# Performance work log

Hardware: AMD Instinct MI355X
Metric: run time of the kernel (lower is better)

Reference implementation:

```python
import jax, jax.numpy as jnp
import numpy as np

COMMITMENT_COST = 0.25


def setup_inputs() -> dict:
    key = jax.random.key(0)
    k1, k2 = jax.random.split(key)
    inputs = jax.random.normal(k1, (64, 1024, 128), dtype=jnp.float32)
    # torch.rand init -> uniform [0, 1)
    codewords = jax.random.uniform(k2, (1024, 128), dtype=jnp.float32)
    return {"inputs": inputs, "codewords": codewords}


def reference(inputs, codewords):
    sg = jax.lax.stop_gradient
    D = codewords.shape[-1]
    flat = inputs.reshape(-1, D)  # (N, D)
    distances = (
        jnp.sum(flat * flat, axis=1, keepdims=True)
        - 2.0 * flat @ codewords.T
        + jnp.sum(codewords * codewords, axis=1)
    )  # (N, K)
    encoding_indices = jnp.argmin(distances, axis=1)  # (N,)
    quantized = codewords[encoding_indices].reshape(inputs.shape)

    quantizing_loss = jnp.mean((sg(quantized) - inputs) ** 2)
    commitment_loss = jnp.mean((quantized - sg(inputs)) ** 2)
    loss = quantizing_loss + COMMITMENT_COST * commitment_loss

    # straight-through estimator
    quantized = inputs + sg(quantized - inputs)
    return quantized, encoding_indices[:, None], loss
```

## Files before the change

### kernel.cpp

```cpp
#include <hip/hip_runtime.h>
#include <stdint.h>


typedef short     bf16x8 __attribute__((ext_vector_type(8)));
typedef float     f32x4  __attribute__((ext_vector_type(4)));
typedef unsigned short u16x8 __attribute__((ext_vector_type(8)));
typedef unsigned short u16x2 __attribute__((ext_vector_type(2)));

constexpr int N_ROWS = 65536;
constexpr int K_CODES = 1024;
constexpr int D = 128;
constexpr float MARGIN = 0.01f;

__device__ __forceinline__ unsigned short f32_to_bf16_rn(float f) {
    unsigned u = __float_as_uint(f);
    unsigned r = (u + 0x7FFFu + ((u >> 16) & 1u)) >> 16;
    return (unsigned short)r;
}
__device__ __forceinline__ float bf16_to_f32(unsigned short h) {
    return __uint_as_float(((unsigned)h) << 16);
}

__device__ __forceinline__ void gload_lds16(const void* g, void* l) {
    __builtin_amdgcn_global_load_lds(
        (const __attribute__((address_space(1))) unsigned int*)g,
        (__attribute__((address_space(3))) unsigned int*)l, 16, 0, 0);
}

__global__ __launch_bounds__(64) void vq_prep_cw(const float* __restrict__ cw,
                                                 unsigned short* __restrict__ Cp,
                                                 float* __restrict__ cnorm,
                                                 int* __restrict__ rcnt,
                                                 double* __restrict__ acc) {
    const int k = blockIdx.x;
    const int lane = threadIdx.x;
    float2 v = reinterpret_cast<const float2*>(cw + (size_t)k * D)[lane];
    float s = v.x * v.x + v.y * v.y;
#pragma unroll
    for (int off = 32; off; off >>= 1) s += __shfl_down(s, off, 64);
    if (lane == 0) cnorm[k] = s;
    if (lane == 0 && k == 0) { *rcnt = 0; *acc = 0.0; }

    unsigned short hx = f32_to_bf16_rn(v.x), hy = f32_to_bf16_rn(v.y);
    unsigned short lx = f32_to_bf16_rn(v.x - bf16_to_f32(hx));
    unsigned short ly = f32_to_bf16_rn(v.y - bf16_to_f32(hy));
    size_t off0 = (size_t)k * D + lane * 2;
    u16x2 hv; hv[0] = hx; hv[1] = hy;
    u16x2 lv; lv[0] = lx; lv[1] = ly;
    *reinterpret_cast<u16x2*>(Cp + off0) = hv;
    *reinterpret_cast<u16x2*>(Cp + 131072 + off0) = lv;
}

__global__ __launch_bounds__(256, 2) void vq_argmin_fused(
    const float* __restrict__ x,
    const unsigned short* __restrict__ Cp,
    const float* __restrict__ cnorm,
    const float* __restrict__ cw,
    float* __restrict__ out_idx_f,
    float* __restrict__ qout,
    float* __restrict__ rowloss,
    float* __restrict__ xnorm,
    int* __restrict__ rcnt,
    int* __restrict__ rrows,
    double* __restrict__ acc) {
    __shared__ unsigned char Bs[2][2][16384];
    __shared__ int idx_s[128];
    __shared__ float xs_n[128];
    __shared__ double wsum[4];

    const int tid = threadIdx.x;
    const int wave = tid >> 6;
    const int lane = tid & 63;
    const int l15 = lane & 15;
    const int lg = lane >> 4;
    const int base = blockIdx.x * 128;
    const int wrow = base + wave * 32;

    const char* Cpb = reinterpret_cast<const char*>(Cp);
    auto stageB = [&](int c, int b) {
#pragma unroll
        for (int u = 0; u < 8; ++u) {
            int t = wave * 8 + u;
            int pl = t >> 4;
            int cwl = (t & 15) * 4 + lg;
            int q = l15 * 16;
            const char* src = Cpb + pl * 262144 + ((size_t)(c * 64 + cwl)) * 256
                              + (q ^ ((cwl & 7) << 4));
            void* dst = (void*)&Bs[b][pl][(t & 15) * 1024];
            gload_lds16(src, dst);
        }
    };
    stageB(0, 0);

    bf16x8 A[2][4][2];
    float xn[2] = {0.f, 0.f};
#pragma unroll
    for (int r2 = 0; r2 < 2; ++r2) {
        const float* xr0 = x + (size_t)(wrow + r2 * 16 + l15) * D;
#pragma unroll
        for (int s = 0; s < 4; ++s) {
            const float4* xf = reinterpret_cast<const float4*>(xr0 + s * 32 + lg * 8);
            float4 f0 = xf[0];
            float4 f1 = xf[1];
            float in[8] = {f0.x, f0.y, f0.z, f0.w, f1.x, f1.y, f1.z, f1.w};
            u16x8 hv, lv;
#pragma unroll
            for (int e = 0; e < 8; ++e) {
                xn[r2] += in[e] * in[e];
                unsigned short h = f32_to_bf16_rn(in[e]);
                hv[e] = h;
                lv[e] = f32_to_bf16_rn(in[e] - bf16_to_f32(h));
            }
            A[r2][s][0] = *reinterpret_cast<bf16x8*>(&hv);
            A[r2][s][1] = *reinterpret_cast<bf16x8*>(&lv);
        }
    }
#pragma unroll
    for (int r2 = 0; r2 < 2; ++r2) {
        xn[r2] += __shfl_xor(xn[r2], 16, 64);
        xn[r2] += __shfl_xor(xn[r2], 32, 64);
        if (lg == 0) {
            xs_n[wave * 32 + r2 * 16 + l15] = xn[r2];
            xnorm[wrow + r2 * 16 + l15] = xn[r2];
        }
    }

    float bv[2][4], bv2[2][4];
    int bi_[2][4];
#pragma unroll
    for (int r2 = 0; r2 < 2; ++r2)
#pragma unroll
        for (int i = 0; i < 4; ++i) { bv[r2][i] = 3.4e38f; bv2[r2][i] = 3.4e38f; bi_[r2][i] = 0; }

    const int cb = l15 * 256;
    const int swz = (l15 & 7) << 4;
    int kb[4];
#pragma unroll
    for (int s = 0; s < 4; ++s) kb[s] = (s * 64 + lg * 16) ^ swz;

    asm volatile("s_waitcnt vmcnt(0)" ::: "memory");
    __syncthreads();

    for (int c = 0; c < 16; ++c) {
        const int buf = c & 1;
        if (c < 15) stageB(c + 1, buf ^ 1);

        f32x4 accf[2][4];
#pragma unroll
        for (int r2 = 0; r2 < 2; ++r2)
#pragma unroll
            for (int j = 0; j < 4; ++j) accf[r2][j] = (f32x4)(0.f);

#pragma unroll
        for (int s = 0; s < 4; ++s) {
            bf16x8 bh[4], bl[4];
#pragma unroll
            for (int j = 0; j < 4; ++j) {
                int ad = j * 4096 + cb + kb[s];
                bh[j] = *reinterpret_cast<const bf16x8*>(&Bs[buf][0][ad]);
                bl[j] = *reinterpret_cast<const bf16x8*>(&Bs[buf][1][ad]);
            }
#pragma unroll
            for (int r2 = 0; r2 < 2; ++r2)
#pragma unroll
                for (int j = 0; j < 4; ++j) {
                    accf[r2][j] = __builtin_amdgcn_mfma_f32_16x16x32_bf16(
                        A[r2][s][0], bh[j], accf[r2][j], 0, 0, 0);
                    accf[r2][j] = __builtin_amdgcn_mfma_f32_16x16x32_bf16(
                        A[r2][s][0], bl[j], accf[r2][j], 0, 0, 0);
                    accf[r2][j] = __builtin_amdgcn_mfma_f32_16x16x32_bf16(
                        A[r2][s][1], bh[j], accf[r2][j], 0, 0, 0);
                }
        }

#pragma unroll
        for (int j = 0; j < 4; ++j) {
            int col = c * 64 + j * 16 + l15;
            float cn = cnorm[col];
#pragma unroll
            for (int r2 = 0; r2 < 2; ++r2)
#pragma unroll
                for (int i = 0; i < 4; ++i) {
                    float sc = cn - 2.f * accf[r2][j][i];
                    if (sc < bv[r2][i]) {
                        bv2[r2][i] = bv[r2][i];
                        bv[r2][i] = sc;
                        bi_[r2][i] = col;
                    } else if (sc < bv2[r2][i]) {
                        bv2[r2][i] = sc;
                    }
                }
        }
        asm volatile("s_waitcnt vmcnt(0)" ::: "memory");
        __syncthreads();
    }

    double lsum = 0.0;
#pragma unroll
    for (int r2 = 0; r2 < 2; ++r2)
#pragma unroll
        for (int i = 0; i < 4; ++i) {
            float v = bv[r2][i], v2 = bv2[r2][i];
            int ix = bi_[r2][i];
#pragma unroll
            for (int off = 1; off < 16; off <<= 1) {
                float ov = __shfl_xor(v, off, 64);
                float ov2 = __shfl_xor(v2, off, 64);
                int oi = __shfl_xor(ix, off, 64);
                float nv2 = fminf(fminf(v2, ov2), fmaxf(v, ov));
                if (ov < v || (ov == v && oi < ix)) { v = ov; ix = oi; }
                v2 = nv2;
            }
            if (l15 == 0) {
                int rl_loc = wave * 32 + r2 * 16 + lg * 4 + i;
                int row = base + rl_loc;
                out_idx_f[row] = (float)ix;
                idx_s[rl_loc] = ix;
                float rl = xs_n[rl_loc] + v;
                rowloss[row] = rl;
                lsum += (double)rl;
                if (v2 - v < MARGIN) {
                    int p = atomicAdd(rcnt, 1);
                    rrows[p] = row;
                }
            }
        }

#pragma unroll
    for (int off = 32; off; off >>= 1) lsum += __shfl_down(lsum, off, 64);
    if (lane == 0) wsum[wave] = lsum;
    __syncthreads();
    if (tid == 0) atomicAdd(acc, wsum[0] + wsum[1] + wsum[2] + wsum[3]);

    const float4* cw4 = reinterpret_cast<const float4*>(cw);
    float4* q4 = reinterpret_cast<float4*>(qout);
#pragma unroll
    for (int it = 0; it < 16; ++it) {
        int i = it * 256 + tid;
        int r = i >> 5, d4 = i & 31;
        q4[(size_t)(base + r) * 32 + d4] = cw4[(size_t)idx_s[r] * 32 + d4];
    }
}

__global__ __launch_bounds__(256) void vq_repair(const float* __restrict__ x,
                                                 const float* __restrict__ cw,
                                                 const float* __restrict__ cnorm,
                                                 const float* __restrict__ xnorm,
                                                 const int* __restrict__ rcnt,
                                                 const int* __restrict__ rrows,
                                                 float* __restrict__ out_idx_f,
                                                 float* __restrict__ qout,
                                                 float* __restrict__ rowloss,
                                                 double* __restrict__ acc) {
    __shared__ float xs[16][132];
    __shared__ int rowids[16];
    __shared__ float sval[16][16];
    __shared__ int sidx[16][16];
    __shared__ int fidx[16];

    const int t = threadIdx.x;
    const int count = *rcnt;
    const float4* cw4 = reinterpret_cast<const float4*>(cw);
    double dsum = 0.0;

    for (int g = blockIdx.x; g * 16 < count; g += 512) {
        int nrows = min(16, count - g * 16);
        __syncthreads();
        if (t < 16) rowids[t] = rrows[g * 16 + (t < nrows ? t : 0)];
        __syncthreads();
        for (int i = t; i < 512; i += 256) {
            int r = i >> 5, d4 = i & 31;
            *reinterpret_cast<float4*>(&xs[r][d4 * 4]) =
                reinterpret_cast<const float4*>(x)[(size_t)rowids[r] * 32 + d4];
        }
        __syncthreads();

        const int r = t & 15;
        const int qq = t >> 4;
        float bv = 3.4e38f;
        int bi = 0;
#pragma unroll 2
        for (int kt = 0; kt < 8; ++kt) {
            float a[8] = {0.f, 0.f, 0.f, 0.f, 0.f, 0.f, 0.f, 0.f};
            int k0 = qq * 64 + kt * 8;
            for (int d4 = 0; d4 < 32; ++d4) {
                float4 xv = *reinterpret_cast<const float4*>(&xs[r][d4 * 4]);
#pragma unroll
                for (int kk = 0; kk < 8; ++kk) {
                    float4 cv = cw4[(size_t)(k0 + kk) * 32 + d4];
                    a[kk] += xv.x * cv.x + xv.y * cv.y + xv.z * cv.z + xv.w * cv.w;
                }
            }
#pragma unroll
            for (int kk = 0; kk < 8; ++kk) {
                int k = k0 + kk;
                float sc = cnorm[k] - 2.f * a[kk];
                if (sc < bv) { bv = sc; bi = k; }
            }
        }
        sval[r][qq] = bv;
        sidx[r][qq] = bi;
        __syncthreads();
        if (t < 16) {
            float fv = sval[t][0];
            int fi = sidx[t][0];
#pragma unroll
            for (int q2 = 1; q2 < 16; ++q2) {
                float v = sval[t][q2];
                int ii = sidx[t][q2];
                if (v < fv || (v == fv && ii < fi)) { fv = v; fi = ii; }
            }
            fidx[t] = fi;
            if (t < nrows) {
                int row = rowids[t];
                out_idx_f[row] = (float)fi;
                float nrl = xnorm[row] + fv;
                float orl = rowloss[row];
                rowloss[row] = nrl;
                dsum += (double)nrl - (double)orl;
            }
        }
        __syncthreads();
        for (int i = t; i < 512; i += 256) {
            int rr = i >> 5, d4 = i & 31;
            float4 q4 = cw4[(size_t)fidx[rr] * 32 + d4];
            reinterpret_cast<float4*>(qout)[(size_t)rowids[rr] * 32 + d4] = q4;
        }
    }
#pragma unroll
    for (int off = 32; off; off >>= 1) dsum += __shfl_down(dsum, off, 64);
    __shared__ double wsum[4];
    if ((t & 63) == 0) wsum[t >> 6] = dsum;
    __syncthreads();
    if (t == 0) {
        double b = wsum[0] + wsum[1] + wsum[2] + wsum[3];
        if (b != 0.0) atomicAdd(acc, b);
    }
}

__global__ void vq_loss_final(const double* __restrict__ acc,
                              float* __restrict__ out_loss) {
    *out_loss = (float)(*acc * (1.25 / (double)((size_t)N_ROWS * D)));
}

extern "C" void kernel_launch(void* const* d_in, const int* in_sizes, int n_in,
                              void* d_out, int out_size, void* d_ws, size_t ws_size,
                              hipStream_t stream) {
    const float* x = (const float*)d_in[0];
    const float* cw = (const float*)d_in[1];

    float* qout = (float*)d_out;
    float* out_idx_f = qout + (size_t)N_ROWS * D;
    float* out_loss = out_idx_f + N_ROWS;

    char* w = (char*)d_ws;
    unsigned short* Cp = (unsigned short*)w;          w += 524288;
    float* cnorm = (float*)w;                         w += 4096;
    int* rcnt = (int*)w;                              w += 16;
    double* acc = (double*)w;                         w += 240;
    int* rrows = (int*)w;                             w += 262144;
    float* xnorm = (float*)w;                         w += 262144;
    float* rowloss = (float*)w;                       w += 262144;

    vq_prep_cw<<<K_CODES, 64, 0, stream>>>(cw, Cp, cnorm, rcnt, acc);
    vq_argmin_fused<<<N_ROWS / 128, 256, 0, stream>>>(
        x, Cp, cnorm, cw, out_idx_f, qout, rowloss, xnorm, rcnt, rrows, acc);
    vq_repair<<<512, 256, 0, stream>>>(
        x, cw, cnorm, xnorm, rcnt, rrows, out_idx_f, qout, rowloss, acc);
    vq_loss_final<<<1, 1, 0, stream>>>(acc, out_loss);
}
```

Baseline: 225.7 us.

## Split codeword columns across two wave groups per block with 512 threads

Doubles the block to 512 threads. Each row group of 4 waves is duplicated, and each copy handles half of every 64-codeword chunk (32 columns). Per-wave top-2 results go through shared memory and are merged by the first 128 threads, which then write the index, loss and repair flags. The aim is more waves per CU and fewer accumulator registers per wave, to raise occupancy and hide MFMA and LDS latency. The cost is that both halves redundantly load and split x into bf16, plus an extra shared-memory merge step and barrier.

```diff
diff --git a/kernel.cpp b/kernel.cpp
--- a/kernel.cpp
+++ b/kernel.cpp
@@ -51,7 +51,7 @@
     *reinterpret_cast<u16x2*>(Cp + 131072 + off0) = lv;
 }
 
-__global__ __launch_bounds__(256, 2) void vq_argmin_fused(
+__global__ __launch_bounds__(512, 4) void vq_argmin_fused(
     const float* __restrict__ x,
     const unsigned short* __restrict__ Cp,
     const float* __restrict__ cnorm,
@@ -64,23 +64,27 @@
     int* __restrict__ rrows,
     double* __restrict__ acc) {
     __shared__ unsigned char Bs[2][2][16384];
+    __shared__ float mv[2][128], mv2[2][128];
+    __shared__ int mi[2][128];
     __shared__ int idx_s[128];
     __shared__ float xs_n[128];
-    __shared__ double wsum[4];
+    __shared__ double wsum[8];
 
     const int tid = threadIdx.x;
     const int wave = tid >> 6;
     const int lane = tid & 63;
     const int l15 = lane & 15;
     const int lg = lane >> 4;
+    const int rg = wave & 3;
+    const int ch = wave >> 2;
     const int base = blockIdx.x * 128;
-    const int wrow = base + wave * 32;
+    const int wrow = base + rg * 32;
 
     const char* Cpb = reinterpret_cast<const char*>(Cp);
     auto stageB = [&](int c, int b) {
 #pragma unroll
-        for (int u = 0; u < 8; ++u) {
-            int t = wave * 8 + u;
+        for (int u = 0; u < 4; ++u) {
+            int t = wave * 4 + u;
             int pl = t >> 4;
             int cwl = (t & 15) * 4 + lg;
             int q = l15 * 16;
@@ -119,18 +123,24 @@
     for (int r2 = 0; r2 < 2; ++r2) {
         xn[r2] += __shfl_xor(xn[r2], 16, 64);
         xn[r2] += __shfl_xor(xn[r2], 32, 64);
-        if (lg == 0) {
-            xs_n[wave * 32 + r2 * 16 + l15] = xn[r2];
+        if (ch == 0 && lg == 0) {
+            xs_n[rg * 32 + r2 * 16 + l15] = xn[r2];
             xnorm[wrow + r2 * 16 + l15] = xn[r2];
         }
     }
 
-    float bv[2][4], bv2[2][4];
-    int bi_[2][4];
+    float bv[2][2], bv2[2][2];
+    int bi_[2][2];
 #pragma unroll
     for (int r2 = 0; r2 < 2; ++r2)
 #pragma unroll
-        for (int i = 0; i < 4; ++i) { bv[r2][i] = 3.4e38f; bv2[r2][i] = 3.4e38f; bi_[r2][i] = 0; }
+        for (int i = 0; i < 2; ++i) {}
+    float tv[2][4], tv2[2][4];
+    int ti[2][4];
+#pragma unroll
+    for (int r2 = 0; r2 < 2; ++r2)
+#pragma unroll
+        for (int i = 0; i < 4; ++i) { tv[r2][i] = 3.4e38f; tv2[r2][i] = 3.4e38f; ti[r2][i] = 0; }
 
     const int cb = l15 * 256;
     const int swz = (l15 & 7) << 4;
@@ -145,25 +155,25 @@
         const int buf = c & 1;
         if (c < 15) stageB(c + 1, buf ^ 1);
 
-        f32x4 accf[2][4];
+        f32x4 accf[2][2];
 #pragma unroll
         for (int r2 = 0; r2 < 2; ++r2)
 #pragma unroll
-            for (int j = 0; j < 4; ++j) accf[r2][j] = (f32x4)(0.f);
+            for (int j = 0; j < 2; ++j) accf[r2][j] = (f32x4)(0.f);
 
 #pragma unroll
         for (int s = 0; s < 4; ++s) {
-            bf16x8 bh[4], bl[4];
-#pragma unroll
-            for (int j = 0; j < 4; ++j) {
-                int ad = j * 4096 + cb + kb[s];
+            bf16x8 bh[2], bl[2];
+#pragma unroll
+            for (int j = 0; j < 2; ++j) {
+                int ad = (ch * 2 + j) * 4096 + cb + kb[s];
                 bh[j] = *reinterpret_cast<const bf16x8*>(&Bs[buf][0][ad]);
                 bl[j] = *reinterpret_cast<const bf16x8*>(&Bs[buf][1][ad]);
             }
 #pragma unroll
             for (int r2 = 0; r2 < 2; ++r2)
 #pragma unroll
-                for (int j = 0; j < 4; ++j) {
+                for (int j = 0; j < 2; ++j) {
                     accf[r2][j] = __builtin_amdgcn_mfma_f32_16x16x32_bf16(
                         A[r2][s][0], bh[j], accf[r2][j], 0, 0, 0);
                     accf[r2][j] = __builtin_amdgcn_mfma_f32_16x16x32_bf16(
@@ -174,20 +184,20 @@
         }
 
 #pragma unroll
-        for (int j = 0; j < 4; ++j) {
-            int col = c * 64 + j * 16 + l15;
+        for (int j = 0; j < 2; ++j) {
+            int col = c * 64 + (ch * 2 + j) * 16 + l15;
             float cn = cnorm[col];
 #pragma unroll
             for (int r2 = 0; r2 < 2; ++r2)
 #pragma unroll
                 for (int i = 0; i < 4; ++i) {
                     float sc = cn - 2.f * accf[r2][j][i];
-                    if (sc < bv[r2][i]) {
-                        bv2[r2][i] = bv[r2][i];
-                        bv[r2][i] = sc;
-                        bi_[r2][i] = col;
-                    } else if (sc < bv2[r2][i]) {
-                        bv2[r2][i] = sc;
+                    if (sc < tv[r2][i]) {
+                        tv2[r2][i] = tv[r2][i];
+                        tv[r2][i] = sc;
+                        ti[r2][i] = col;
+                    } else if (sc < tv2[r2][i]) {
+                        tv2[r2][i] = sc;
                     }
                 }
         }
@@ -195,13 +205,12 @@
         __syncthreads();
     }
 
-    double lsum = 0.0;
 #pragma unroll
     for (int r2 = 0; r2 < 2; ++r2)
 #pragma unroll
         for (int i = 0; i < 4; ++i) {
-            float v = bv[r2][i], v2 = bv2[r2][i];
-            int ix = bi_[r2][i];
+            float v = tv[r2][i], v2 = tv2[r2][i];
+            int ix = ti[r2][i];
 #pragma unroll
             for (int off = 1; off < 16; off <<= 1) {
                 float ov = __shfl_xor(v, off, 64);
@@ -212,31 +221,53 @@
                 v2 = nv2;
             }
             if (l15 == 0) {
-                int rl_loc = wave * 32 + r2 * 16 + lg * 4 + i;
-                int row = base + rl_loc;
-                out_idx_f[row] = (float)ix;
-                idx_s[rl_loc] = ix;
-                float rl = xs_n[rl_loc] + v;
-                rowloss[row] = rl;
-                lsum += (double)rl;
-                if (v2 - v < MARGIN) {
-                    int p = atomicAdd(rcnt, 1);
-                    rrows[p] = row;
-                }
-            }
-        }
+                int rl = rg * 32 + r2 * 16 + lg * 4 + i;
+                mv[ch][rl] = v;
+                mv2[ch][rl] = v2;
+                mi[ch][rl] = ix;
+            }
+        }
+    __syncthreads();
+
+    double lsum = 0.0;
+    if (tid < 128) {
+        int row = base + tid;
+        float v0 = mv[0][tid], v0b = mv2[0][tid];
+        int i0 = mi[0][tid];
+        float v1 = mv[1][tid], v1b = mv2[1][tid];
+        int i1 = mi[1][tid];
+        bool take0 = (v0 < v1) || (v0 == v1 && i0 <= i1);
+        float best = take0 ? v0 : v1;
+        int bidx = take0 ? i0 : i1;
+        float second = take0 ? fminf(v1, v0b) : fminf(v0, v1b);
+
+        out_idx_f[row] = (float)bidx;
+        idx_s[tid] = bidx;
+        float rl = xs_n[tid] + best;
+        rowloss[row] = rl;
+        lsum = (double)rl;
+        if (second - best < MARGIN) {
+            int p = atomicAdd(rcnt, 1);
+            rrows[p] = row;
+        }
+    }
 
 #pragma unroll
     for (int off = 32; off; off >>= 1) lsum += __shfl_down(lsum, off, 64);
     if (lane == 0) wsum[wave] = lsum;
     __syncthreads();
-    if (tid == 0) atomicAdd(acc, wsum[0] + wsum[1] + wsum[2] + wsum[3]);
+    if (tid == 0) {
+        double b = 0.0;
+#pragma unroll
+        for (int q = 0; q < 8; ++q) b += wsum[q];
+        atomicAdd(acc, b);
+    }
 
     const float4* cw4 = reinterpret_cast<const float4*>(cw);
     float4* q4 = reinterpret_cast<float4*>(qout);
 #pragma unroll
-    for (int it = 0; it < 16; ++it) {
-        int i = it * 256 + tid;
+    for (int it = 0; it < 8; ++it) {
+        int i = it * 512 + tid;
         int r = i >> 5, d4 = i & 31;
         q4[(size_t)(base + r) * 32 + d4] = cw4[(size_t)idx_s[r] * 32 + d4];
     }
@@ -363,7 +394,7 @@
     float* rowloss = (float*)w;                       w += 262144;
 
     vq_prep_cw<<<K_CODES, 64, 0, stream>>>(cw, Cp, cnorm, rcnt, acc);
-    vq_argmin_fused<<<N_ROWS / 128, 256, 0, stream>>>(
+    vq_argmin_fused<<<N_ROWS / 128, 512, 0, stream>>>(
         x, Cp, cnorm, cw, out_idx_f, qout, rowloss, xnorm, rcnt, rrows, acc);
     vq_repair<<<512, 256, 0, stream>>>(
         x, cw, cnorm, xnorm, rcnt, rrows, out_idx_f, qout, rowloss, acc);
```

After: 253.8 us. +12.4%, slower.
